# Kernel optimization log

Hardware: AMD Instinct MI355X
Metric: run time of the kernel (lower is better)

Reference implementation:

```python
import jax, jax.numpy as jnp
import numpy as np

HIDDEN = 1024
RANK = 4
N_TASKS = 5
LORA_SCALING = 1.0 / RANK  # lora_alpha / lora_rank = 1/4
LN_EPS = 1e-5


def setup_inputs() -> dict:
    key = jax.random.key(0)
    ks = jax.random.split(key, 9)
    B, S, D = 16, 2048, HIDDEN
    hidden_states = jax.random.normal(ks[0], (B, S, D), dtype=jnp.float32)
    input_tensor = jax.random.normal(ks[1], (B, S, D), dtype=jnp.float32)
    adapter_mask = jax.random.randint(ks[2], (B,), 0, N_TASKS, dtype=jnp.int32)
    W = jax.random.normal(ks[3], (D, D), dtype=jnp.float32) * 0.02
    b = jax.random.normal(ks[4], (D,), dtype=jnp.float32) * 0.02
    lora_A = jax.random.normal(ks[5], (N_TASKS, RANK, D), dtype=jnp.float32) * 0.02
    lora_B = jax.random.normal(ks[6], (N_TASKS, D, RANK), dtype=jnp.float32) * 0.02
    gamma = jnp.ones((D,), dtype=jnp.float32)
    beta = jnp.zeros((D,), dtype=jnp.float32)
    return {
        "hidden_states": hidden_states,
        "input_tensor": input_tensor,
        "W": W,
        "b": b,
        "lora_A": lora_A,
        "lora_B": lora_B,
        "gamma": gamma,
        "beta": beta,
        "adapter_mask": adapter_mask,
    }


def _layernorm(x, gamma, beta):
    mu = jnp.mean(x, axis=-1, keepdims=True)
    xc = x - mu
    var = jnp.mean(xc * xc, axis=-1, keepdims=True)
    return xc * jax.lax.rsqrt(var + LN_EPS) * gamma + beta


def reference(hidden_states, input_tensor, W, b, lora_A, lora_B, gamma, beta, adapter_mask):
    # Base dense projection (first self.dense call)
    h1 = jnp.einsum("bsd,ed->bse", hidden_states, W) + b  # [B,S,D]
    # Per-task LoRA-parametrized dense applied to the projected states
    # (the source loops over unique tasks with gather/scatter; vectorized here
    #  by gathering each batch row's adapter).
    base2 = jnp.einsum("bsd,ed->bse", h1, W) + b  # [B,S,D]
    A_b = lora_A[adapter_mask]  # [B, r, D]
    B_b = lora_B[adapter_mask]  # [B, D, r]
    low = jnp.einsum("bsd,brd->bsr", h1, A_b)  # [B,S,r]
    delta = jnp.einsum("bsr,bdr->bsd", low, B_b)  # [B,S,D]
    h2 = base2 + LORA_SCALING * delta
    # dropout is identity in eval / p=0; residual + LayerNorm
    return _layernorm(h2 + input_tensor, gamma, beta)
```

## Files before the change

### kernel.cpp

```cpp
#include <hip/hip_runtime.h>
#include <hip/hip_bf16.h>
#include <stdint.h>

#define D_HID 1024
#define M_TOT 32768
#define LN_EPS 1e-5f

typedef __bf16 bf16x8 __attribute__((ext_vector_type(8)));
typedef float f32x4 __attribute__((ext_vector_type(4)));
typedef unsigned short u16;
typedef u16 u16x8 __attribute__((ext_vector_type(8)));
typedef u16 u16x4v __attribute__((ext_vector_type(4)));

__device__ __forceinline__ float bf2f(u16 x) {
  union { unsigned int u; float f; } c; c.u = ((unsigned int)x) << 16; return c.f;
}
__device__ __forceinline__ u16 f2bf(float f) {
  union { __bf16 h; u16 u; } c; c.h = (__bf16)f; return c.u;
}
__device__ __forceinline__ void gld16(const u16* g, u16* lds_wave_base) {
  __builtin_amdgcn_global_load_lds(
      (__attribute__((address_space(1))) unsigned int*)g,
      (__attribute__((address_space(3))) unsigned int*)lds_wave_base, 16, 0, 0);
}

__global__ __launch_bounds__(256) void s1_prep(
    const float* __restrict__ hs, u16* __restrict__ hs_bf,
    const float* __restrict__ W, u16* __restrict__ hi, u16* __restrict__ lo,
    u16* __restrict__ hiT, u16* __restrict__ loT,
    const float* __restrict__ lA, u16* __restrict__ lAh, u16* __restrict__ lAl) {
  __shared__ float tile[32][33];
  const int bid = blockIdx.x, tid = threadIdx.x;
  if (bid < 16384) {
    const size_t idx = (size_t)bid * 256 + tid;
    const float4 a = *(const float4*)(hs + idx * 8);
    const float4 b = *(const float4*)(hs + idx * 8 + 4);
    u16x8 o;
    o[0] = f2bf(a.x); o[1] = f2bf(a.y); o[2] = f2bf(a.z); o[3] = f2bf(a.w);
    o[4] = f2bf(b.x); o[5] = f2bf(b.y); o[6] = f2bf(b.z); o[7] = f2bf(b.w);
    *(u16x8*)(hs_bf + idx * 8) = o;
    return;
  }
  if (bid >= 17408) {
    const int b = bid - 17408;
    for (int i = tid; i < 16 * 1024; i += 256) {
      const int r = b * 16 + (i >> 10), c = i & 1023;
      const float v = (r < 20) ? lA[(size_t)r * 1024 + c] : 0.f;
      const u16 h = f2bf(v);
      lAh[(size_t)r * 1024 + c] = h;
      lAl[(size_t)r * 1024 + c] = f2bf(v - bf2f(h));
    }
    return;
  }
  const int rb = bid - 16384;
  const int bj = rb & 31, bi = rb >> 5;
  const int tx = tid & 31, ty = tid >> 5;
#pragma unroll
  for (int r0 = 0; r0 < 32; r0 += 8) {
    const int r = r0 + ty;
    const size_t o = (size_t)(bi * 32 + r) * D_HID + bj * 32 + tx;
    const float v = W[o];
    tile[r][tx] = v;
    const u16 h = f2bf(v);
    hi[o] = h; lo[o] = f2bf(v - bf2f(h));
  }
  __syncthreads();
#pragma unroll
  for (int r0 = 0; r0 < 32; r0 += 8) {
    const int r = r0 + ty;
    const float v = tile[tx][r];
    const size_t o = (size_t)(bj * 32 + r) * D_HID + bi * 32 + tx;
    const u16 h = f2bf(v);
    hiT[o] = h; loT[o] = f2bf(v - bf2f(h));
  }
}

__global__ __launch_bounds__(256) void s2_gemm(
    const u16* __restrict__ Ah, const u16* __restrict__ Al,
    const u16* __restrict__ Bh, const u16* __restrict__ Bl,
    const u16* __restrict__ lAh, const u16* __restrict__ lAl,
    float* __restrict__ C, float* __restrict__ A2) {
  __shared__ __align__(16) u16 smem[4][64 * 32];
  const int bid = blockIdx.x, tid = threadIdx.x;
  const int wave = tid >> 6, lane = tid & 63;
  const int by = bid >> 4, bx = bid & 15;
  const bool isA2 = (by == 16);
  const u16* Asel_h = isA2 ? lAh : Ah;
  const u16* Asel_l = isA2 ? lAl : Al;
  const int arow0 = isA2 ? 0 : by * 64;
  const u16* gsel = (wave == 0) ? Asel_h : (wave == 1) ? Asel_l
                  : (wave == 2) ? Bh : Bl;
  const int rb = (wave < 2) ? arow0 : bx * 64;
  const u16* gp = gsel + (size_t)(rb + (lane >> 2)) * D_HID + (lane & 3) * 8;
  u16* sb = &smem[wave][0];

  const int l15 = lane & 15, quad = lane >> 4;
  const int wm = wave >> 1, wn = wave & 1;
  const int fA = (wm * 32 + l15) * 32 + quad * 8;
  const int fB = (wn * 32 + l15) * 32 + quad * 8;
  f32x4 acc[2][2];
#pragma unroll
  for (int m = 0; m < 2; ++m)
#pragma unroll
    for (int n = 0; n < 2; ++n) acc[m][n] = (f32x4){0.f, 0.f, 0.f, 0.f};

  for (int k0 = 0; k0 < D_HID; k0 += 32) {
    __syncthreads();
#pragma unroll
    for (int q = 0; q < 4; ++q)
      gld16(gp + (size_t)q * 16 * D_HID, sb + q * 512);
    gp += 32;
    __syncthreads();
    bf16x8 ahf[2], alf[2], bhf[2], blf[2];
#pragma unroll
    for (int m = 0; m < 2; ++m) {
      ahf[m] = *(const bf16x8*)(&smem[0][fA + m * 512]);
      alf[m] = *(const bf16x8*)(&smem[1][fA + m * 512]);
    }
#pragma unroll
    for (int n = 0; n < 2; ++n) {
      bhf[n] = *(const bf16x8*)(&smem[2][fB + n * 512]);
      blf[n] = *(const bf16x8*)(&smem[3][fB + n * 512]);
    }
#pragma unroll
    for (int m = 0; m < 2; ++m)
#pragma unroll
      for (int n = 0; n < 2; ++n) {
        acc[m][n] = __builtin_amdgcn_mfma_f32_16x16x32_bf16(ahf[m], bhf[n], acc[m][n], 0, 0, 0);
        acc[m][n] = __builtin_amdgcn_mfma_f32_16x16x32_bf16(alf[m], bhf[n], acc[m][n], 0, 0, 0);
        acc[m][n] = __builtin_amdgcn_mfma_f32_16x16x32_bf16(ahf[m], blf[n], acc[m][n], 0, 0, 0);
      }
  }
  const int nn0 = bx * 64 + wn * 32;
#pragma unroll
  for (int m = 0; m < 2; ++m)
#pragma unroll
    for (int n = 0; n < 2; ++n) {
      const int nn = nn0 + n * 16 + l15;
#pragma unroll
      for (int r = 0; r < 4; ++r) {
        const int lr = wm * 32 + m * 16 + quad * 4 + r;
        if (!isA2) {
          C[(size_t)(by * 64 + lr) * D_HID + nn] = acc[m][n][r];
        } else if (lr < 20) {
          A2[(size_t)lr * D_HID + nn] = acc[m][n][r];
        }
      }
    }
}

__global__ __launch_bounds__(256) void weff_beff(
    const float* __restrict__ Wc, const float* __restrict__ A2,
    const float* __restrict__ lB, const float* __restrict__ lA,
    const float* __restrict__ W, const float* __restrict__ bvec,
    u16* __restrict__ Weff, float* __restrict__ beff) {
  const int n = blockIdx.x, t = blockIdx.y, tid = threadIdx.x;
  const int wave = tid >> 6, lane = tid & 63;
  float br[4];
#pragma unroll
  for (int r = 0; r < 4; ++r) br[r] = lB[(size_t)t * 4096 + n * 4 + r];
  float4 v = *(const float4*)(Wc + (size_t)n * D_HID + tid * 4);
#pragma unroll
  for (int r = 0; r < 4; ++r) {
    const float4 a2 = *(const float4*)(A2 + (size_t)(t * 4 + r) * D_HID + tid * 4);
    const float s = 0.25f * br[r];
    v.x += s * a2.x; v.y += s * a2.y; v.z += s * a2.z; v.w += s * a2.w;
  }
  u16x4v o; o[0] = f2bf(v.x); o[1] = f2bf(v.y); o[2] = f2bf(v.z); o[3] = f2bf(v.w);
  *(u16x4v*)(Weff + (size_t)t * 1048576 + (size_t)n * D_HID + tid * 4) = o;
  const float4 bb = *(const float4*)(bvec + tid * 4);
  float p[5];
  {
    const float4 wr = *(const float4*)(W + (size_t)n * D_HID + tid * 4);
    p[0] = wr.x * bb.x + wr.y * bb.y + wr.z * bb.z + wr.w * bb.w;
  }
#pragma unroll
  for (int r = 0; r < 4; ++r) {
    const float4 ar = *(const float4*)(lA + (size_t)(t * 4 + r) * D_HID + tid * 4);
    p[1 + r] = ar.x * bb.x + ar.y * bb.y + ar.z * bb.z + ar.w * bb.w;
  }
#pragma unroll
  for (int m = 1; m < 64; m <<= 1)
#pragma unroll
    for (int jj = 0; jj < 5; ++jj) p[jj] += __shfl_xor(p[jj], m);
  __shared__ float red[4][5];
  if (lane == 0)
#pragma unroll
    for (int jj = 0; jj < 5; ++jj) red[wave][jj] = p[jj];
  __syncthreads();
  if (tid == 0) {
    float P = 0.f, Cr[4] = {0.f, 0.f, 0.f, 0.f};
#pragma unroll
    for (int w = 0; w < 4; ++w) {
      P += red[w][0];
#pragma unroll
      for (int r = 0; r < 4; ++r) Cr[r] += red[w][1 + r];
    }
    const float e = br[0]*Cr[0] + br[1]*Cr[1] + br[2]*Cr[2] + br[3]*Cr[3];
    beff[t * D_HID + n] = P + bvec[n] + 0.25f * e;
  }
}

__global__ __launch_bounds__(512, 1) void gemm_main(
    const u16* __restrict__ Ag, const u16* __restrict__ Wf,
    const float* __restrict__ beff, const int* __restrict__ mask,
    float* __restrict__ out) {
  __shared__ __align__(16) u16 sAf[2 * 16384];
  __shared__ __align__(16) u16 sBf[2 * 16384];
  const int tid = threadIdx.x, wave = tid >> 6, lane = tid & 63;
  const int L = blockIdx.x;
  const int xcd = L & 7, j = L >> 3;
  const int bx = j & 3;
  const int by = xcd * 16 + (j >> 2);
  const int task = mask[by >> 3];
  const u16* Bg = Wf + (size_t)task * (D_HID * D_HID);

  const int acol = ((lane & 7) ^ (lane >> 3)) * 8;
  const int aBase = (by * 256 + wave * 8 + (lane >> 3)) * D_HID + acol;
  const int bBase = (bx * 256 + wave * 8 + (lane >> 3)) * D_HID + acol;

  auto stageA = [&](int ktar, int half) {
#pragma unroll
    for (int q = 0; q < 2; ++q)
      gld16(Ag + (aBase + ktar * 64 + half * 131072 + q * 65536),
            sAf + ((ktar & 1) * 16384 + half * 8192 + q * 4096 + wave * 512));
  };
  auto stageB = [&](int ktar, int half) {
#pragma unroll
    for (int q = 0; q < 2; ++q)
      gld16(Bg + (bBase + ktar * 64 + half * 131072 + q * 65536),
            sBf + ((ktar & 1) * 16384 + half * 8192 + q * 4096 + wave * 512));
  };

  const int wm = wave >> 2, wn = wave & 3;
  const int l15 = lane & 15, quad = lane >> 4, l7 = lane & 7;
  const int vA0 = (wm * 128 + l15) * 64 + ((quad ^ l7) * 8);
  const int vB0 = (wn * 64 + l15) * 64 + ((quad ^ l7) * 8);

  f32x4 acc[8][4];
#pragma unroll
  for (int i = 0; i < 8; ++i)
#pragma unroll
    for (int jn = 0; jn < 4; ++jn) acc[i][jn] = (f32x4){0.f, 0.f, 0.f, 0.f};

  stageB(0, 0); stageB(0, 1); stageA(0, 0); stageA(0, 1);
  stageB(1, 0); stageA(1, 0);
  asm volatile("s_waitcnt vmcnt(4)" ::: "memory");
  __builtin_amdgcn_s_barrier();
  __builtin_amdgcn_sched_barrier(0);

  bf16x8 a[4][2], b[4][2];
#pragma unroll 1
  for (int k2 = 0; k2 < 8; ++k2) {
#pragma unroll
    for (int par = 0; par < 2; ++par) {
      const int kt = k2 * 2 + par;
      const u16* pA = sAf + par * 16384;
      const u16* pB = sBf + par * 16384;
      const bool st01 = (par == 0) || (k2 < 7);
      const bool st23 = (k2 < 7);

#pragma unroll
      for (int m4 = 0; m4 < 4; ++m4) {
        a[m4][0] = *(const bf16x8*)(pA + (vA0 + m4 * 1024));
        a[m4][1] = *(const bf16x8*)(pA + ((vA0 ^ 32) + m4 * 1024));
      }
#pragma unroll
      for (int n2 = 0; n2 < 2; ++n2) {
        b[n2][0] = *(const bf16x8*)(pB + (vB0 + n2 * 1024));
        b[n2][1] = *(const bf16x8*)(pB + ((vB0 ^ 32) + n2 * 1024));
      }
      if (st01) stageB(kt + 1, 1);
      __builtin_amdgcn_s_barrier();
      asm volatile("s_waitcnt lgkmcnt(0)" ::: "memory");
      __builtin_amdgcn_sched_barrier(0);
      __builtin_amdgcn_s_setprio(1);
#pragma unroll
      for (int m4 = 0; m4 < 4; ++m4)
#pragma unroll
        for (int n2 = 0; n2 < 2; ++n2)
#pragma unroll
          for (int kk = 0; kk < 2; ++kk)
            acc[m4][n2] = __builtin_amdgcn_mfma_f32_16x16x32_bf16(
                a[m4][kk], b[n2][kk], acc[m4][n2], 0, 0, 0);
      __builtin_amdgcn_s_setprio(0);
      __builtin_amdgcn_s_barrier();
      __builtin_amdgcn_sched_barrier(0);

#pragma unroll
      for (int n2 = 0; n2 < 2; ++n2) {
        b[2 + n2][0] = *(const bf16x8*)(pB + (vB0 + (2 + n2) * 1024));
        b[2 + n2][1] = *(const bf16x8*)(pB + ((vB0 ^ 32) + (2 + n2) * 1024));
      }
      if (st01) stageA(kt + 1, 1);
      __builtin_amdgcn_s_barrier();
      asm volatile("s_waitcnt lgkmcnt(0)" ::: "memory");
      __builtin_amdgcn_sched_barrier(0);
      __builtin_amdgcn_s_setprio(1);
#pragma unroll
      for (int m4 = 0; m4 < 4; ++m4)
#pragma unroll
        for (int n2 = 0; n2 < 2; ++n2)
#pragma unroll
          for (int kk = 0; kk < 2; ++kk)
            acc[m4][2 + n2] = __builtin_amdgcn_mfma_f32_16x16x32_bf16(
                a[m4][kk], b[2 + n2][kk], acc[m4][2 + n2], 0, 0, 0);
      __builtin_amdgcn_s_setprio(0);
      __builtin_amdgcn_s_barrier();
      __builtin_amdgcn_sched_barrier(0);

#pragma unroll
      for (int m4 = 0; m4 < 4; ++m4) {
        a[m4][0] = *(const bf16x8*)(pA + (vA0 + (4 + m4) * 1024));
        a[m4][1] = *(const bf16x8*)(pA + ((vA0 ^ 32) + (4 + m4) * 1024));
      }
      if (st23) stageB(kt + 2, 0);
      __builtin_amdgcn_s_barrier();
      asm volatile("s_waitcnt lgkmcnt(0)" ::: "memory");
      __builtin_amdgcn_sched_barrier(0);
      __builtin_amdgcn_s_setprio(1);
#pragma unroll
      for (int m4 = 0; m4 < 4; ++m4)
#pragma unroll
        for (int n2 = 0; n2 < 2; ++n2)
#pragma unroll
          for (int kk = 0; kk < 2; ++kk)
            acc[4 + m4][n2] = __builtin_amdgcn_mfma_f32_16x16x32_bf16(
                a[m4][kk], b[n2][kk], acc[4 + m4][n2], 0, 0, 0);
      __builtin_amdgcn_s_setprio(0);
      __builtin_amdgcn_s_barrier();
      __builtin_amdgcn_sched_barrier(0);

      if (st23) stageA(kt + 2, 0);
      if (par == 0) {
        if (k2 < 7) { asm volatile("s_waitcnt vmcnt(4)" ::: "memory"); }
        else        { asm volatile("s_waitcnt vmcnt(0)" ::: "memory"); }
      } else {
        if (k2 < 7) { asm volatile("s_waitcnt vmcnt(4)" ::: "memory"); }
      }
      __builtin_amdgcn_s_barrier();
      asm volatile("s_waitcnt lgkmcnt(0)" ::: "memory");
      __builtin_amdgcn_sched_barrier(0);
      __builtin_amdgcn_s_setprio(1);
#pragma unroll
      for (int m4 = 0; m4 < 4; ++m4)
#pragma unroll
        for (int n2 = 0; n2 < 2; ++n2)
#pragma unroll
          for (int kk = 0; kk < 2; ++kk)
            acc[4 + m4][2 + n2] = __builtin_amdgcn_mfma_f32_16x16x32_bf16(
                a[m4][kk], b[2 + n2][kk], acc[4 + m4][2 + n2], 0, 0, 0);
      __builtin_amdgcn_s_setprio(0);
      __builtin_amdgcn_s_barrier();
      __builtin_amdgcn_sched_barrier(0);
    }
  }

  const float* bb = beff + task * D_HID;
  const size_t mBase = (size_t)by * 256 + wm * 128;
  const int nb0 = bx * 256 + wn * 64;
#pragma unroll
  for (int mf = 0; mf < 8; ++mf)
#pragma unroll
    for (int nf = 0; nf < 4; ++nf) {
      const int n = nb0 + nf * 16 + l15;
      const float bval = bb[n];
#pragma unroll
      for (int r = 0; r < 4; ++r) {
        const size_t m = mBase + mf * 16 + quad * 4 + r;
        out[m * D_HID + n] = acc[mf][nf][r] + bval;
      }
    }
}

__global__ __launch_bounds__(256) void ln4(float* __restrict__ io,
                                           const float* __restrict__ resid,
                                           const float* __restrict__ gamma,
                                           const float* __restrict__ beta) {
  const int row = blockIdx.x * 4 + (threadIdx.x >> 6);
  const int lane = threadIdx.x & 63;
  float* p = io + (size_t)row * D_HID + lane * 4;
  const float* rp = resid + (size_t)row * D_HID + lane * 4;
  float4 v[4];
#pragma unroll
  for (int k = 0; k < 4; ++k) {
    const float4 h = *(const float4*)(p + k * 256);
    const float4 r = *(const float4*)(rp + k * 256);
    v[k].x = h.x + r.x; v[k].y = h.y + r.y;
    v[k].z = h.z + r.z; v[k].w = h.w + r.w;
  }
  float s = 0.f, q = 0.f;
#pragma unroll
  for (int k = 0; k < 4; ++k) {
    s += v[k].x + v[k].y + v[k].z + v[k].w;
    q += v[k].x * v[k].x + v[k].y * v[k].y + v[k].z * v[k].z + v[k].w * v[k].w;
  }
#pragma unroll
  for (int m = 1; m < 64; m <<= 1) { s += __shfl_xor(s, m); q += __shfl_xor(q, m); }
  const float mu  = s * (1.f / (float)D_HID);
  const float var = q * (1.f / (float)D_HID) - mu * mu;
  const float inv = rsqrtf(var + LN_EPS);
#pragma unroll
  for (int k = 0; k < 4; ++k) {
    const float4 g  = *(const float4*)(gamma + lane * 4 + k * 256);
    const float4 bb = *(const float4*)(beta + lane * 4 + k * 256);
    float4 o;
    o.x = (v[k].x - mu) * inv * g.x + bb.x;
    o.y = (v[k].y - mu) * inv * g.y + bb.y;
    o.z = (v[k].z - mu) * inv * g.z + bb.z;
    o.w = (v[k].w - mu) * inv * g.w + bb.w;
    *(float4*)(p + k * 256) = o;
  }
}

extern "C" void kernel_launch(void* const* d_in, const int* in_sizes, int n_in,
                              void* d_out, int out_size, void* d_ws, size_t ws_size,
                              hipStream_t stream) {
  const float* hs    = (const float*)d_in[0];
  const float* inp   = (const float*)d_in[1];
  const float* W     = (const float*)d_in[2];
  const float* b     = (const float*)d_in[3];
  const float* lA    = (const float*)d_in[4];
  const float* lB    = (const float*)d_in[5];
  const float* gamma = (const float*)d_in[6];
  const float* beta  = (const float*)d_in[7];
  const int*   mask  = (const int*)d_in[8];
  float* out = (float*)d_out;

  char* wsb = (char*)d_ws;
  u16*   hs_bf = (u16*)wsb;
  float* Wc    = (float*)(wsb + 67108864);
  u16*   weff  = (u16*)(wsb + 71303168);
  u16*   Whi   = weff;
  u16*   Wlo   = weff + 1048576;
  u16*   WhiT  = weff + 2097152;
  u16*   WloT  = weff + 3145728;
  u16*   lAh   = weff + 4194304;
  u16*   lAl   = weff + 4325376;
  float* A2    = (float*)(wsb + 81788928);
  float* beff  = (float*)(wsb + 81871360);

  s1_prep<<<17416, 256, 0, stream>>>(hs, hs_bf, W, Whi, Wlo, WhiT, WloT, lA, lAh, lAl);
  s2_gemm<<<272, 256, 0, stream>>>(Whi, Wlo, WhiT, WloT, lAh, lAl, Wc, A2);
  weff_beff<<<dim3(1024, 5), 256, 0, stream>>>(Wc, A2, lB, lA, W, b, weff, beff);
  gemm_main<<<512, 512, 0, stream>>>(hs_bf, weff, beff, mask, out);
  ln4<<<M_TOT / 4, 256, 0, stream>>>(out, inp, gamma, beta);
}
```

Before: 485.6 us.

## Spread hidden-state bf16 conversion across the three prep kernels to overlap work

```diff
diff --git a/kernel.cpp b/kernel.cpp
--- a/kernel.cpp
+++ b/kernel.cpp
@@ -24,25 +24,35 @@
       (__attribute__((address_space(3))) unsigned int*)lds_wave_base, 16, 0, 0);
 }
 
-__global__ __launch_bounds__(256) void s1_prep(
+__device__ __forceinline__ void cvt_job(const float* __restrict__ hs,
+                                        u16* __restrict__ hs_bf, size_t idx) {
+  const float4 a = *(const float4*)(hs + idx * 8);
+  const float4 b = *(const float4*)(hs + idx * 8 + 4);
+  u16x8 o;
+  o[0] = f2bf(a.x); o[1] = f2bf(a.y); o[2] = f2bf(a.z); o[3] = f2bf(a.w);
+  o[4] = f2bf(b.x); o[5] = f2bf(b.y); o[6] = f2bf(b.z); o[7] = f2bf(b.w);
+  *(u16x8*)(hs_bf + idx * 8) = o;
+}
+
+#define CVT_K1_BLKS 5440
+#define CVT_K2_BLKS 5472
+#define CVT_K3_BLKS 5472
+#define CVT_K2_OFF  (CVT_K1_BLKS * 256)
+#define CVT_K3_OFF  ((CVT_K1_BLKS + CVT_K2_BLKS) * 256)
+
+__global__ __launch_bounds__(256) void k1_prep(
     const float* __restrict__ hs, u16* __restrict__ hs_bf,
     const float* __restrict__ W, u16* __restrict__ hi, u16* __restrict__ lo,
     u16* __restrict__ hiT, u16* __restrict__ loT,
     const float* __restrict__ lA, u16* __restrict__ lAh, u16* __restrict__ lAl) {
   __shared__ float tile[32][33];
   const int bid = blockIdx.x, tid = threadIdx.x;
-  if (bid < 16384) {
-    const size_t idx = (size_t)bid * 256 + tid;
-    const float4 a = *(const float4*)(hs + idx * 8);
-    const float4 b = *(const float4*)(hs + idx * 8 + 4);
-    u16x8 o;
-    o[0] = f2bf(a.x); o[1] = f2bf(a.y); o[2] = f2bf(a.z); o[3] = f2bf(a.w);
-    o[4] = f2bf(b.x); o[5] = f2bf(b.y); o[6] = f2bf(b.z); o[7] = f2bf(b.w);
-    *(u16x8*)(hs_bf + idx * 8) = o;
+  if (bid >= 1032) {
+    cvt_job(hs, hs_bf, (size_t)(bid - 1032) * 256 + tid);
     return;
   }
-  if (bid >= 17408) {
-    const int b = bid - 17408;
+  if (bid >= 1024) {
+    const int b = bid - 1024;
     for (int i = tid; i < 16 * 1024; i += 256) {
       const int r = b * 16 + (i >> 10), c = i & 1023;
       const float v = (r < 20) ? lA[(size_t)r * 1024 + c] : 0.f;
@@ -52,8 +62,7 @@
     }
     return;
   }
-  const int rb = bid - 16384;
-  const int bj = rb & 31, bi = rb >> 5;
+  const int bj = bid & 31, bi = bid >> 5;
   const int tx = tid & 31, ty = tid >> 5;
 #pragma unroll
   for (int r0 = 0; r0 < 32; r0 += 8) {
@@ -75,13 +84,18 @@
   }
 }
 
-__global__ __launch_bounds__(256) void s2_gemm(
+__global__ __launch_bounds__(256) void k2_s2(
     const u16* __restrict__ Ah, const u16* __restrict__ Al,
     const u16* __restrict__ Bh, const u16* __restrict__ Bl,
     const u16* __restrict__ lAh, const u16* __restrict__ lAl,
+    const float* __restrict__ hs, u16* __restrict__ hs_bf,
     float* __restrict__ C, float* __restrict__ A2) {
   __shared__ __align__(16) u16 smem[4][64 * 32];
   const int bid = blockIdx.x, tid = threadIdx.x;
+  if (bid >= 272) {
+    cvt_job(hs, hs_bf, (size_t)CVT_K2_OFF + (size_t)(bid - 272) * 256 + tid);
+    return;
+  }
   const int wave = tid >> 6, lane = tid & 63;
   const int by = bid >> 4, bx = bid & 15;
   const bool isA2 = (by == 16);
@@ -149,12 +163,18 @@
     }
 }
 
-__global__ __launch_bounds__(256) void weff_beff(
+__global__ __launch_bounds__(256) void k3_weff(
     const float* __restrict__ Wc, const float* __restrict__ A2,
     const float* __restrict__ lB, const float* __restrict__ lA,
     const float* __restrict__ W, const float* __restrict__ bvec,
+    const float* __restrict__ hs, u16* __restrict__ hs_bf,
     u16* __restrict__ Weff, float* __restrict__ beff) {
-  const int n = blockIdx.x, t = blockIdx.y, tid = threadIdx.x;
+  const int bid = blockIdx.x, tid = threadIdx.x;
+  if (bid >= 5120) {
+    cvt_job(hs, hs_bf, (size_t)CVT_K3_OFF + (size_t)(bid - 5120) * 256 + tid);
+    return;
+  }
+  const int n = bid & 1023, t = bid >> 10;
   const int wave = tid >> 6, lane = tid & 63;
   float br[4];
 #pragma unroll
@@ -440,9 +460,12 @@
   float* A2    = (float*)(wsb + 81788928);
   float* beff  = (float*)(wsb + 81871360);
 
-  s1_prep<<<17416, 256, 0, stream>>>(hs, hs_bf, W, Whi, Wlo, WhiT, WloT, lA, lAh, lAl);
-  s2_gemm<<<272, 256, 0, stream>>>(Whi, Wlo, WhiT, WloT, lAh, lAl, Wc, A2);
-  weff_beff<<<dim3(1024, 5), 256, 0, stream>>>(Wc, A2, lB, lA, W, b, weff, beff);
+  k1_prep<<<1032 + CVT_K1_BLKS, 256, 0, stream>>>(
+      hs, hs_bf, W, Whi, Wlo, WhiT, WloT, lA, lAh, lAl);
+  k2_s2<<<272 + CVT_K2_BLKS, 256, 0, stream>>>(
+      Whi, Wlo, WhiT, WloT, lAh, lAl, hs, hs_bf, Wc, A2);
+  k3_weff<<<5120 + CVT_K3_BLKS, 256, 0, stream>>>(
+      Wc, A2, lB, lA, W, b, hs, hs_bf, weff, beff);
   gemm_main<<<512, 512, 0, stream>>>(hs_bf, weff, beff, mask, out);
   ln4<<<M_TOT / 4, 256, 0, stream>>>(out, inp, gamma, beta);
 }
```

Measured after the change: 478.6 us. No clear change (-1.5%).
